# Kernel tuning notes

Hardware: AMD Instinct MI355X
Metric: run time of the kernel (lower is better)

## Reference

```python
import jax, jax.numpy as jnp
import numpy as np

INPUT_SIZE, HIDDEN, N, T = 124, 64, 4096, 64


def setup_inputs() -> dict:
    key = jax.random.key(0)
    ks = jax.random.split(key, 12)
    s = 1.0 / np.sqrt(HIDDEN)  # PyTorch RNN init: U(-1/sqrt(h), 1/sqrt(h))
    u = lambda k, shape: jax.random.uniform(k, shape, jnp.float32, -s, s)
    return {
        "x": jax.random.normal(ks[0], (N, T, INPUT_SIZE), jnp.float32),
        "W_ih0": u(ks[1], (HIDDEN, INPUT_SIZE)),
        "W_hh0": u(ks[2], (HIDDEN, HIDDEN)),
        "b_ih0": u(ks[3], (HIDDEN,)),
        "b_hh0": u(ks[4], (HIDDEN,)),
        "W_ih1": u(ks[5], (HIDDEN, HIDDEN)),
        "W_hh1": u(ks[6], (HIDDEN, HIDDEN)),
        "b_ih1": u(ks[7], (HIDDEN,)),
        "b_hh1": u(ks[8], (HIDDEN,)),
        "W_fc": u(ks[9], (1, HIDDEN)),
        "b_fc": u(ks[10], (1,)),
    }


def reference(x, W_ih0, W_hh0, b_ih0, b_hh0, W_ih1, W_hh1, b_ih1, b_hh1, W_fc, b_fc):
    # 2-layer tanh RNN (batch_first), eval mode (dropout inactive).
    # Precompute layer-0 input projections for all timesteps: [T, N, H]
    xproj = jnp.einsum("ntf,hf->tnh", x, W_ih0) + b_ih0
    h0 = jnp.zeros((x.shape[0], HIDDEN), x.dtype)
    h1 = jnp.zeros((x.shape[0], HIDDEN), x.dtype)

    def step(carry, xp_t):
        h0, h1 = carry
        h0 = jnp.tanh(xp_t + h0 @ W_hh0.T + b_hh0)
        h1 = jnp.tanh(h0 @ W_ih1.T + b_ih1 + h1 @ W_hh1.T + b_hh1)
        return (h0, h1), None

    (h0, h1), _ = jax.lax.scan(step, (h0, h1), xproj)
    # out[:, -1, :] of top layer == final h1; linear head to scalar
    return (h1 @ W_fc.T + b_fc).squeeze(-1)  # [N]
```

## Files before the change

kernel.cpp:

```cpp
#include <hip/hip_runtime.h>
#include <stdint.h>


typedef float  f32x4 __attribute__((ext_vector_type(4)));
typedef short  s16x8 __attribute__((ext_vector_type(8)));
typedef unsigned int u32;
typedef unsigned int u32x4 __attribute__((ext_vector_type(4)));

#define TSTEPS 64
#define FIN    124
#define HID    64

__device__ __forceinline__ f32x4 zero4() {
  f32x4 z = {0.f, 0.f, 0.f, 0.f};
  return z;
}

__device__ __forceinline__ void split8(const f32x4 a, const f32x4 b,
                                       s16x8& hi, s16x8& lo) {
  float e[8] = {a[0], a[1], a[2], a[3], b[0], b[1], b[2], b[3]};
  u32x4 hu, lu;
#pragma unroll
  for (int p = 0; p < 4; ++p) {
    u32 u0 = __float_as_uint(e[2 * p]);
    u32 u1 = __float_as_uint(e[2 * p + 1]);
    u32 h0b = u0 & 0xFFFF0000u;
    u32 h1b = u1 & 0xFFFF0000u;
    hu[p] = (u0 >> 16) | h1b;
    float r0 = e[2 * p]     - __uint_as_float(h0b);
    float r1 = e[2 * p + 1] - __uint_as_float(h1b);
    lu[p] = (__float_as_uint(r0) >> 16) | (__float_as_uint(r1) & 0xFFFF0000u);
  }
  hi = __builtin_bit_cast(s16x8, hu);
  lo = __builtin_bit_cast(s16x8, lu);
}

__device__ __forceinline__ f32x4 MFMA(s16x8 a, s16x8 b, f32x4 c) {
  return __builtin_amdgcn_mfma_f32_16x16x32_bf16(a, b, c, 0, 0, 0);
}

__device__ __forceinline__ float tanh_f(float x) {
  x = fminf(15.f, fmaxf(-15.f, x));
  float e = __builtin_amdgcn_exp2f(x * 2.88539008177793f);
  return (e - 1.f) * __builtin_amdgcn_rcpf(e + 1.f);
}

__global__ __launch_bounds__(256, 1) void rnn2_fused_kernel(
    const float* __restrict__ x,
    const float* __restrict__ Wih0, const float* __restrict__ Whh0,
    const float* __restrict__ bih0, const float* __restrict__ bhh0,
    const float* __restrict__ Wih1, const float* __restrict__ Whh1,
    const float* __restrict__ bih1, const float* __restrict__ bhh1,
    const float* __restrict__ Wfc,  const float* __restrict__ bfc,
    float* __restrict__ out) {
  __shared__ __align__(16) unsigned short XH[2][16][136];
  __shared__ __align__(16) unsigned short XL[2][16][136];
  __shared__ __align__(16) unsigned short S0H[2][16][72];
  __shared__ __align__(16) unsigned short S0L[2][16][72];
  __shared__ __align__(16) unsigned short S1H[2][16][72];
  __shared__ __align__(16) unsigned short S1L[2][16][72];
  __shared__ float WFC[64];
  __shared__ float RED[64];

  const int tid  = (int)threadIdx.x;
  const int lane = tid & 63;
  const int wv   = tid >> 6;
  const int r16  = lane & 15;
  const int g    = lane >> 4;
  const int col  = 16 * wv + r16;
  const int n0   = (int)blockIdx.x * 16;

  s16x8 WH[3][2][2];
  {
    const float* Wp[3] = {Whh0, Wih1, Whh1};
#pragma unroll
    for (int p = 0; p < 3; ++p) {
#pragma unroll
      for (int c = 0; c < 2; ++c) {
        const float* base = Wp[p] + col * HID + 32 * c + 8 * g;
        f32x4 a = *(const f32x4*)base;
        f32x4 b = *(const f32x4*)(base + 4);
        split8(a, b, WH[p][c][0], WH[p][c][1]);
      }
    }
  }
  s16x8 WI[4][2];
#pragma unroll
  for (int c = 0; c < 4; ++c) {
    const float* base = Wih0 + col * FIN + 32 * c + 8 * g;
    f32x4 a = *(const f32x4*)base;
    f32x4 b = zero4();
    if (!(c == 3 && g == 3)) b = *(const f32x4*)(base + 4);
    split8(a, b, WI[c][0], WI[c][1]);
  }

  const float bias0 = bih0[col] + bhh0[col];
  const float bias1 = bih1[col] + bhh1[col];

  {
    u32* z0 = (u32*)&S0H[0][0][0];
    u32* z1 = (u32*)&S0L[0][0][0];
    u32* z2 = (u32*)&S1H[0][0][0];
    u32* z3 = (u32*)&S1L[0][0][0];
    for (int i = tid; i < 16 * 72 / 2; i += 256) {
      z0[i] = 0; z1[i] = 0; z2[i] = 0; z3[i] = 0;
    }
  }
  if (tid < 64) WFC[tid] = Wfc[tid];

  const int xr = tid >> 4;
  const int xs = tid & 15;
  const float* xrow = x + (size_t)(n0 + xr) * (TSTEPS * FIN);
  f32x4 xa, xb;
  {
    const float* b0 = xrow + 8 * xs;
    xa = *(const f32x4*)b0;
    xb = zero4();
    if (xs != 15) xb = *(const f32x4*)(b0 + 4);
    s16x8 fh, fl;
    split8(xa, xb, fh, fl);
    *(s16x8*)&XH[0][xr][8 * xs] = fh;
    *(s16x8*)&XL[0][xr][8 * xs] = fl;
  }
  {
    const float* b1 = xrow + FIN + 8 * xs;
    xa = *(const f32x4*)b1;
    xb = zero4();
    if (xs != 15) xb = *(const f32x4*)(b1 + 4);
  }
  __syncthreads();

#pragma unroll 2
  for (int t = 0; t < TSTEPS; ++t) {
    const int P = t & 1;

    {
      s16x8 fh, fl;
      split8(xa, xb, fh, fl);
      *(s16x8*)&XH[1 - P][xr][8 * xs] = fh;
      *(s16x8*)&XL[1 - P][xr][8 * xs] = fl;
    }
    {
      int t2 = (t + 2 < TSTEPS) ? (t + 2) : (TSTEPS - 1);
      const float* bp = xrow + t2 * FIN + 8 * xs;
      xa = *(const f32x4*)bp;
      xb = zero4();
      if (xs != 15) xb = *(const f32x4*)(bp + 4);
    }

    s16x8 h0h[2], h0l[2], xh[4], xl[4], h1h[2], h1l[2];
#pragma unroll
    for (int c = 0; c < 2; ++c) {
      h0h[c] = *(const s16x8*)&S0H[P][r16][32 * c + 8 * g];
      h0l[c] = *(const s16x8*)&S0L[P][r16][32 * c + 8 * g];
      h1h[c] = *(const s16x8*)&S1H[P][r16][32 * c + 8 * g];
      h1l[c] = *(const s16x8*)&S1L[P][r16][32 * c + 8 * g];
    }
#pragma unroll
    for (int c = 0; c < 4; ++c) {
      xh[c] = *(const s16x8*)&XH[P][r16][32 * c + 8 * g];
      xl[c] = *(const s16x8*)&XL[P][r16][32 * c + 8 * g];
    }

    f32x4 a0 = {bias0, bias0, bias0, bias0};
    f32x4 a1 = zero4();
    f32x4 a2 = zero4();
    f32x4 a3 = zero4();
    f32x4 a4 = zero4();
    f32x4 a5 = zero4();
    f32x4 b0 = {bias1, bias1, bias1, bias1};
    f32x4 b1 = zero4();

    a0 = MFMA(h0h[0], WH[0][0][0], a0);
    a1 = MFMA(h0h[0], WH[0][0][1], a1);
    a2 = MFMA(h0l[0], WH[0][0][0], a2);
    a3 = MFMA(xh[2], WI[2][0], a3);
    a4 = MFMA(xh[2], WI[2][1], a4);
    a5 = MFMA(xl[2], WI[2][0], a5);
    b0 = MFMA(h1h[0], WH[2][0][0], b0);
    b1 = MFMA(h1l[0], WH[2][0][0], b1);

    a0 = MFMA(h0h[1], WH[0][1][0], a0);
    a1 = MFMA(h0h[1], WH[0][1][1], a1);
    a2 = MFMA(h0l[1], WH[0][1][0], a2);
    a3 = MFMA(xh[3], WI[3][0], a3);
    a4 = MFMA(xh[3], WI[3][1], a4);
    a5 = MFMA(xl[3], WI[3][0], a5);
    b0 = MFMA(h1h[1], WH[2][1][0], b0);
    b1 = MFMA(h1l[1], WH[2][1][0], b1);

    a0 = MFMA(xh[0], WI[0][0], a0);
    a1 = MFMA(xh[0], WI[0][1], a1);
    a2 = MFMA(xl[0], WI[0][0], a2);
    b0 = MFMA(h1h[0], WH[2][0][1], b0);

    a0 = MFMA(xh[1], WI[1][0], a0);
    a1 = MFMA(xh[1], WI[1][1], a1);
    a2 = MFMA(xl[1], WI[1][0], a2);
    b0 = MFMA(h1h[1], WH[2][1][1], b0);

#pragma unroll
    for (int i = 0; i < 4; ++i) {
      float h = tanh_f(((a0[i] + a1[i]) + (a2[i] + a3[i])) + (a4[i] + a5[i]));
      u32 u  = __float_as_uint(h);
      u32 hb = u & 0xFFFF0000u;
      S0H[1 - P][4 * g + i][col] = (unsigned short)(u >> 16);
      float rl = h - __uint_as_float(hb);
      S0L[1 - P][4 * g + i][col] = (unsigned short)(__float_as_uint(rl) >> 16);
    }
    __syncthreads();

    f32x4 b2 = zero4();
    f32x4 b3 = zero4();
#pragma unroll
    for (int c = 0; c < 2; ++c) {
      s16x8 ah = *(const s16x8*)&S0H[1 - P][r16][32 * c + 8 * g];
      s16x8 al = *(const s16x8*)&S0L[1 - P][r16][32 * c + 8 * g];
      b2 = MFMA(ah, WH[1][c][0], b2);
      b3 = MFMA(al, WH[1][c][0], b3);
      b2 = MFMA(ah, WH[1][c][1], b2);
    }
#pragma unroll
    for (int i = 0; i < 4; ++i) {
      float h = tanh_f((b0[i] + b1[i]) + (b2[i] + b3[i]));
      u32 u  = __float_as_uint(h);
      u32 hb = u & 0xFFFF0000u;
      S1H[1 - P][4 * g + i][col] = (unsigned short)(u >> 16);
      float rl = h - __uint_as_float(hb);
      S1L[1 - P][4 * g + i][col] = (unsigned short)(__float_as_uint(rl) >> 16);
    }
    __syncthreads();
  }

  if (tid < 64) {
    const int r = tid & 15;
    const int q = tid >> 4;
    float acc = 0.f;
#pragma unroll
    for (int k = 0; k < 16; ++k) {
      int kk = 16 * q + k;
      float hv = __uint_as_float(((u32)S1H[0][r][kk]) << 16) +
                 __uint_as_float(((u32)S1L[0][r][kk]) << 16);
      acc += hv * WFC[kk];
    }
    RED[tid] = acc;
  }
  __syncthreads();
  if (tid < 16) {
    float o = RED[tid] + RED[tid + 16] + RED[tid + 32] + RED[tid + 48] + bfc[0];
    out[n0 + tid] = o;
  }
}

extern "C" void kernel_launch(void* const* d_in, const int* in_sizes, int n_in,
                              void* d_out, int out_size, void* d_ws,
                              size_t ws_size, hipStream_t stream) {
  (void)in_sizes; (void)n_in; (void)d_ws; (void)ws_size; (void)out_size;
  const float* x    = (const float*)d_in[0];
  const float* Wih0 = (const float*)d_in[1];
  const float* Whh0 = (const float*)d_in[2];
  const float* bih0 = (const float*)d_in[3];
  const float* bhh0 = (const float*)d_in[4];
  const float* Wih1 = (const float*)d_in[5];
  const float* Whh1 = (const float*)d_in[6];
  const float* bih1 = (const float*)d_in[7];
  const float* bhh1 = (const float*)d_in[8];
  const float* Wfc  = (const float*)d_in[9];
  const float* bfc  = (const float*)d_in[10];

  rnn2_fused_kernel<<<256, 256, 0, stream>>>(
      x, Wih0, Whh0, bih0, bhh0, Wih1, Whh1, bih1, bhh1, Wfc, bfc,
      (float*)d_out);
}
```

Baseline: 262.2 us.

## Use LDS-only barriers, round-to-nearest bf16 splits, and a cheaper tanh

Replaces __syncthreads with a barrier that waits only on LDS/scalar memory counters (lgkmcnt), so the in-flight prefetch of the next x timestep does not have to finish at every step. The truncating hi/lo bf16 split is swapped for HIP's round-to-nearest bf16 conversions. tanh becomes 1 - 2/(e+1) computed with one FMA and no input clamp. Round-to-nearest conversion may cost more instructions than a mask, and dropping the clamp relies on exp2 overflowing to inf, which still gives a correct saturated result.

```diff
diff --git a/kernel.cpp b/kernel.cpp
--- a/kernel.cpp
+++ b/kernel.cpp
@@ -1,11 +1,11 @@
 #include <hip/hip_runtime.h>
+#include <hip/hip_bf16.h>
 #include <stdint.h>
 
 
 typedef float  f32x4 __attribute__((ext_vector_type(4)));
 typedef short  s16x8 __attribute__((ext_vector_type(8)));
 typedef unsigned int u32;
-typedef unsigned int u32x4 __attribute__((ext_vector_type(4)));
 
 #define TSTEPS 64
 #define FIN    124
@@ -16,23 +16,27 @@
   return z;
 }
 
+__device__ __forceinline__ void barrier_lds() {
+  asm volatile("s_waitcnt lgkmcnt(0)" ::: "memory");
+  __builtin_amdgcn_s_barrier();
+  asm volatile("" ::: "memory");
+}
+
 __device__ __forceinline__ void split8(const f32x4 a, const f32x4 b,
                                        s16x8& hi, s16x8& lo) {
   float e[8] = {a[0], a[1], a[2], a[3], b[0], b[1], b[2], b[3]};
-  u32x4 hu, lu;
-#pragma unroll
-  for (int p = 0; p < 4; ++p) {
-    u32 u0 = __float_as_uint(e[2 * p]);
-    u32 u1 = __float_as_uint(e[2 * p + 1]);
-    u32 h0b = u0 & 0xFFFF0000u;
-    u32 h1b = u1 & 0xFFFF0000u;
-    hu[p] = (u0 >> 16) | h1b;
-    float r0 = e[2 * p]     - __uint_as_float(h0b);
-    float r1 = e[2 * p + 1] - __uint_as_float(h1b);
-    lu[p] = (__float_as_uint(r0) >> 16) | (__float_as_uint(r1) & 0xFFFF0000u);
-  }
-  hi = __builtin_bit_cast(s16x8, hu);
-  lo = __builtin_bit_cast(s16x8, lu);
+  s16x8 h, l;
+#pragma unroll
+  for (int p = 0; p < 8; ++p) {
+    float v = e[p];
+    __hip_bfloat16 bh = __float2bfloat16(v);
+    float r = v - __bfloat162float(bh);
+    __hip_bfloat16 bl = __float2bfloat16(r);
+    h[p] = (short)__builtin_bit_cast(unsigned short, bh);
+    l[p] = (short)__builtin_bit_cast(unsigned short, bl);
+  }
+  hi = h;
+  lo = l;
 }
 
 __device__ __forceinline__ f32x4 MFMA(s16x8 a, s16x8 b, f32x4 c) {
@@ -40,9 +44,8 @@
 }
 
 __device__ __forceinline__ float tanh_f(float x) {
-  x = fminf(15.f, fmaxf(-15.f, x));
-  float e = __builtin_amdgcn_exp2f(x * 2.88539008177793f);
-  return (e - 1.f) * __builtin_amdgcn_rcpf(e + 1.f);
+  float e = __builtin_amdgcn_exp2f(x * 2.885390081777927f);
+  return __builtin_fmaf(-2.f, __builtin_amdgcn_rcpf(e + 1.f), 1.f);
 }
 
 __global__ __launch_bounds__(256, 1) void rnn2_fused_kernel(
@@ -128,7 +131,7 @@
     xb = zero4();
     if (xs != 15) xb = *(const f32x4*)(b1 + 4);
   }
-  __syncthreads();
+  barrier_lds();
 
 #pragma unroll 2
   for (int t = 0; t < TSTEPS; ++t) {
@@ -202,13 +205,13 @@
 #pragma unroll
     for (int i = 0; i < 4; ++i) {
       float h = tanh_f(((a0[i] + a1[i]) + (a2[i] + a3[i])) + (a4[i] + a5[i]));
-      u32 u  = __float_as_uint(h);
-      u32 hb = u & 0xFFFF0000u;
-      S0H[1 - P][4 * g + i][col] = (unsigned short)(u >> 16);
-      float rl = h - __uint_as_float(hb);
-      S0L[1 - P][4 * g + i][col] = (unsigned short)(__float_as_uint(rl) >> 16);
-    }
-    __syncthreads();
+      __hip_bfloat16 bh = __float2bfloat16(h);
+      float rl = h - __bfloat162float(bh);
+      __hip_bfloat16 bl = __float2bfloat16(rl);
+      S0H[1 - P][4 * g + i][col] = __builtin_bit_cast(unsigned short, bh);
+      S0L[1 - P][4 * g + i][col] = __builtin_bit_cast(unsigned short, bl);
+    }
+    barrier_lds();
 
     f32x4 b2 = zero4();
     f32x4 b3 = zero4();
@@ -223,13 +226,13 @@
 #pragma unroll
     for (int i = 0; i < 4; ++i) {
       float h = tanh_f((b0[i] + b1[i]) + (b2[i] + b3[i]));
-      u32 u  = __float_as_uint(h);
-      u32 hb = u & 0xFFFF0000u;
-      S1H[1 - P][4 * g + i][col] = (unsigned short)(u >> 16);
-      float rl = h - __uint_as_float(hb);
-      S1L[1 - P][4 * g + i][col] = (unsigned short)(__float_as_uint(rl) >> 16);
-    }
-    __syncthreads();
+      __hip_bfloat16 bh = __float2bfloat16(h);
+      float rl = h - __bfloat162float(bh);
+      __hip_bfloat16 bl = __float2bfloat16(rl);
+      S1H[1 - P][4 * g + i][col] = __builtin_bit_cast(unsigned short, bh);
+      S1L[1 - P][4 * g + i][col] = __builtin_bit_cast(unsigned short, bl);
+    }
+    barrier_lds();
   }
 
   if (tid < 64) {
@@ -245,7 +248,7 @@
     }
     RED[tid] = acc;
   }
-  __syncthreads();
+  barrier_lds();
   if (tid < 16) {
     float o = RED[tid] + RED[tid + 16] + RED[tid + 32] + RED[tid + 48] + bfc[0];
     out[n0 + tid] = o;
```

Result: faster. 222.4 us (-15.2%).
